# Kernel optimization log

Hardware: AMD Instinct MI355X
Metric: run time of the kernel (lower is better)

Reference implementation:

```python
import jax, jax.numpy as jnp
import numpy as np

B, N = 32, 64
ATTR, STATE, REL, GDIM = 4, 8, 4, 32
NF = 128

def _ln(x, w, b, eps=1e-5):
    mu = jnp.mean(x, axis=-1, keepdims=True)
    var = jnp.mean((x - mu) ** 2, axis=-1, keepdims=True)
    return (x - mu) * jax.lax.rsqrt(var + eps) * w + b

def setup_inputs() -> dict:
    key = jax.random.key(0)
    ks = iter(jax.random.split(key, 32))
    d = {}
    d['attrs'] = jax.random.normal(next(ks), (B, N, ATTR), jnp.float32)
    d['states'] = jax.random.normal(next(ks), (B, N, STATE), jnp.float32)
    d['actions'] = jnp.zeros((B, N, 4), jnp.float32)  # action=False, unused
    d['rel_attrs'] = jax.random.normal(next(ks), (B, N, N, REL), jnp.float32)
    def w(shape):
        return jax.random.normal(next(ks), shape, jnp.float32) * 0.05
    d['oe_w0'] = w((NF, ATTR + STATE)); d['oe_b0'] = jnp.zeros((NF,), jnp.float32)
    d['oe_w1'] = w((NF, NF));            d['oe_b1'] = jnp.zeros((NF,), jnp.float32)
    d['re_w0'] = w((NF, STATE + REL + 2 * ATTR)); d['re_b0'] = jnp.zeros((NF,), jnp.float32)
    d['re_w1'] = w((NF, NF));            d['re_b1'] = jnp.zeros((NF,), jnp.float32)
    d['rp_w'] = w((NF, NF + 2 * NF));    d['rp_b'] = jnp.zeros((NF,), jnp.float32)
    d['rp_lnw'] = jnp.ones((NF,), jnp.float32); d['rp_lnb'] = jnp.zeros((NF,), jnp.float32)
    d['pp_w'] = w((NF, 2 * NF));         d['pp_b'] = jnp.zeros((NF,), jnp.float32)
    d['pp_lnw'] = jnp.ones((NF,), jnp.float32); d['pp_lnb'] = jnp.zeros((NF,), jnp.float32)
    d['pr_w0'] = w((NF, NF));            d['pr_b0'] = jnp.zeros((NF,), jnp.float32)
    d['pr_w1'] = w((GDIM, NF));          d['pr_b1'] = jnp.zeros((GDIM,), jnp.float32)
    d['pstep'] = 2
    return d

def reference(attrs, states, actions, rel_attrs,
              oe_w0, oe_b0, oe_w1, oe_b1,
              re_w0, re_b0, re_w1, re_b1,
              rp_w, rp_b, rp_lnw, rp_lnb,
              pp_w, pp_b, pp_lnw, pp_lnb,
              pr_w0, pr_b0, pr_w1, pr_b1, pstep):
    lin = lambda x, w, b: jnp.einsum('...i,oi->...o', x, w) + b
    # ---- encode nodes: [B,N,attr+state] -> [B,N,NF] (action=False) ----
    obj_in = jnp.concatenate([attrs, states], axis=2)
    obj_encode = jax.nn.relu(lin(jax.nn.relu(lin(obj_in, oe_w0, oe_b0)), oe_w1, oe_b1))
    # ---- encode edges over dense N x N pairs ----
    rel_states = states[:, :, None, :] - states[:, None, :, :]        # B,N,N,state
    recv_attr = jnp.broadcast_to(attrs[:, :, None, :], (attrs.shape[0], attrs.shape[1], attrs.shape[1], attrs.shape[2]))
    send_attr = jnp.broadcast_to(attrs[:, None, :, :], recv_attr.shape)
    rel_in = jnp.concatenate([rel_attrs, rel_states, recv_attr, send_attr], axis=3)
    rel_encode = jax.nn.relu(lin(jax.nn.relu(lin(rel_in, re_w0, re_b0)), re_w1, re_b1))  # B,N,N,NF
    # ---- propagation steps ----
    for _ in range(pstep):
        sh = rel_encode.shape[:3] + (obj_encode.shape[-1],)
        recv = jnp.broadcast_to(obj_encode[:, :, None, :], sh)
        send = jnp.broadcast_to(obj_encode[:, None, :, :], sh)
        rel_effect = jax.nn.relu(_ln(lin(jnp.concatenate([rel_encode, recv, send], axis=3), rp_w, rp_b), rp_lnw, rp_lnb))
        rel_agg = rel_effect.sum(axis=2)                               # B,N,NF
        obj_encode = jax.nn.relu(_ln(lin(jnp.concatenate([obj_encode, rel_agg], axis=2), pp_w, pp_b), pp_lnw, pp_lnb))
    # ---- predict + tanh (state_encoder has tanh=True) ----
    out = lin(jax.nn.relu(lin(obj_encode, pr_w0, pr_b0)), pr_w1, pr_b1)
    return jnp.tanh(out)
```

## Files before the change

kernel.cpp:

```cpp
#include <hip/hip_runtime.h>


#define ROWS 2048
typedef unsigned short u16;
typedef unsigned int u32;
typedef __attribute__((ext_vector_type(8))) short bf16x8;
typedef __attribute__((ext_vector_type(4))) float f32x4;

__device__ __forceinline__ float bsu(u16 u) { return __uint_as_float(((u32)u) << 16); }
__device__ __forceinline__ u16 f2b(float f) {
    u32 u = __float_as_uint(f);
    u32 r = (u + 0x7fffu + ((u >> 16) & 1u)) >> 16;
    return (u16)r;
}

__global__ __launch_bounds__(256)
void k_prep(const float* __restrict__ re_w1, const float* __restrict__ rp_w,
            const float* __restrict__ oe_w1, const float* __restrict__ pp_w,
            const float* __restrict__ pr_w0, const float* __restrict__ pr_w1,
            u16* __restrict__ wbfA, u16* __restrict__ wbfB,
            u16* __restrict__ oe_w1b, u16* __restrict__ wrecvb, u16* __restrict__ wsendb,
            u16* __restrict__ pp_wb, u16* __restrict__ pr_w0b, u16* __restrict__ pr_w1b)
{
    int idx = blockIdx.x * 256 + threadIdx.x;
    if (idx < 17408) { int r = idx / 136, c = idx - r * 136;
        wbfA[idx] = f2b(c < 128 ? re_w1[r * 128 + c] : 0.f); return; }
    idx -= 17408;
    if (idx < 17408) { int r = idx / 136, c = idx - r * 136;
        wbfB[idx] = f2b(c < 128 ? rp_w[r * 384 + c] : 0.f); return; }
    idx -= 17408;
    if (idx < 16384) { oe_w1b[idx] = f2b(oe_w1[idx]); return; }
    idx -= 16384;
    if (idx < 16384) { int r = idx >> 7, c = idx & 127;
        wrecvb[idx] = f2b(rp_w[r * 384 + 128 + c]); return; }
    idx -= 16384;
    if (idx < 16384) { int r = idx >> 7, c = idx & 127;
        wsendb[idx] = f2b(rp_w[r * 384 + 256 + c]); return; }
    idx -= 16384;
    if (idx < 32768) { pp_wb[idx] = f2b(pp_w[idx]); return; }
    idx -= 32768;
    if (idx < 16384) { pr_w0b[idx] = f2b(pr_w0[idx]); return; }
    idx -= 16384;
    if (idx < 4096)  { pr_w1b[idx] = f2b(pr_w1[idx]); }
}

__global__ __launch_bounds__(256)
void k_node(const float* __restrict__ attrs, const float* __restrict__ states,
            const float* __restrict__ oe_w0, const float* __restrict__ oe_b0,
            const u16* __restrict__ oe_w1b, const float* __restrict__ oe_b1,
            const float* __restrict__ re_w0, const float* __restrict__ re_b0,
            const u16* __restrict__ wrecvb, const u16* __restrict__ wsendb,
            const float* __restrict__ rp_b,
            u16* __restrict__ objb, float* __restrict__ nr, float* __restrict__ ns,
            float* __restrict__ recvT, float* __restrict__ sendT)
{
    const int r0 = blockIdx.x * 16;
    const int t = threadIdx.x;
    __shared__ float xs[16][12];
    __shared__ float w0s[1536];
    __shared__ float rw0s[2560];
    __shared__ __align__(16) u16 hb[16 * 136];
    __shared__ __align__(16) u16 ob[16 * 136];

    if (t < 192) { int row = t / 12, c = t - row * 12;
        xs[row][c] = (c < 4) ? attrs[(r0 + row) * 4 + c] : states[(r0 + row) * 8 + (c - 4)]; }
    for (int i = t; i < 1536; i += 256) w0s[i] = oe_w0[i];
    for (int i = t; i < 2560; i += 256) rw0s[i] = re_w0[i];
    __syncthreads();

    for (int e = t; e < 2048; e += 256) {
        int row = e >> 7, o = e & 127;
        float h = oe_b0[o];
#pragma unroll
        for (int k = 0; k < 12; k++) h += w0s[o * 12 + k] * xs[row][k];
        hb[row * 136 + o] = f2b(fmaxf(h, 0.f));
        float s0 = 0.f, a0 = 0.f, a1 = 0.f;
#pragma unroll
        for (int k = 0; k < 8; k++) s0 += rw0s[o * 20 + 4 + k] * xs[row][4 + k];
#pragma unroll
        for (int k = 0; k < 4; k++) {
            a0 += rw0s[o * 20 + 12 + k] * xs[row][k];
            a1 += rw0s[o * 20 + 16 + k] * xs[row][k];
        }
        nr[(r0 + row) * 128 + o] = s0 + a0 + re_b0[o];
        ns[(r0 + row) * 128 + o] = a1 - s0;
    }
    __syncthreads();

    const int wave = t >> 6, lane = t & 63, tx = lane & 15, quad = lane >> 4;

    bf16x8 afr[4];
#pragma unroll
    for (int kk = 0; kk < 4; kk++) afr[kk] = *(const bf16x8*)&hb[tx * 136 + kk * 32 + quad * 8];
    f32x4 acc[2]; acc[0] = (f32x4){0.f,0.f,0.f,0.f}; acc[1] = acc[0];
#pragma unroll
    for (int ot = 0; ot < 2; ot++) {
        int o = (wave * 2 + ot) * 16 + tx;
#pragma unroll
        for (int kk = 0; kk < 4; kk++) {
            bf16x8 bfr = *(const bf16x8*)&oe_w1b[o * 128 + kk * 32 + quad * 8];
            acc[ot] = __builtin_amdgcn_mfma_f32_16x16x32_bf16(afr[kk], bfr, acc[ot], 0, 0, 0);
        }
    }
#pragma unroll
    for (int ot = 0; ot < 2; ot++) {
        int o = (wave * 2 + ot) * 16 + tx;
        float bia = oe_b1[o];
#pragma unroll
        for (int r = 0; r < 4; r++)
            ob[(quad * 4 + r) * 136 + o] = f2b(fmaxf(acc[ot][r] + bia, 0.f));
    }
    __syncthreads();
    { int m = t >> 4, c = t & 15;
      *(uint4*)&objb[(r0 + m) * 128 + c * 8] = *(const uint4*)&ob[m * 136 + c * 8]; }

#pragma unroll
    for (int kk = 0; kk < 4; kk++) afr[kk] = *(const bf16x8*)&ob[tx * 136 + kk * 32 + quad * 8];
    f32x4 ar[2], an[2];
    ar[0] = (f32x4){0.f,0.f,0.f,0.f}; ar[1] = ar[0]; an[0] = ar[0]; an[1] = ar[0];
#pragma unroll
    for (int ot = 0; ot < 2; ot++) {
        int o = (wave * 2 + ot) * 16 + tx;
#pragma unroll
        for (int kk = 0; kk < 4; kk++) {
            bf16x8 br = *(const bf16x8*)&wrecvb[o * 128 + kk * 32 + quad * 8];
            ar[ot] = __builtin_amdgcn_mfma_f32_16x16x32_bf16(afr[kk], br, ar[ot], 0, 0, 0);
            bf16x8 bs = *(const bf16x8*)&wsendb[o * 128 + kk * 32 + quad * 8];
            an[ot] = __builtin_amdgcn_mfma_f32_16x16x32_bf16(afr[kk], bs, an[ot], 0, 0, 0);
        }
    }
#pragma unroll
    for (int ot = 0; ot < 2; ot++) {
        int o = (wave * 2 + ot) * 16 + tx;
        float rb = rp_b[o];
#pragma unroll
        for (int r = 0; r < 4; r++) {
            recvT[(r0 + quad * 4 + r) * 128 + o] = ar[ot][r] + rb;
            sendT[(r0 + quad * 4 + r) * 128 + o] = an[ot][r];
        }
    }
}

__global__ __launch_bounds__(256)
void k_edge_enc(const float* __restrict__ rel_attrs,
                const float* __restrict__ re_w0, const u16* __restrict__ wbf,
                const float* __restrict__ re_b1,
                const float* __restrict__ nr, const float* __restrict__ ns,
                u16* __restrict__ relE)
{
    const int blk = blockIdx.x;
    const int b = blk >> 6;
    const int t = threadIdx.x;
    __shared__ __align__(16) u16 wlds[128 * 136];
    __shared__ __align__(16) u16 albuf[64 * 136];
    __shared__ float nrs[128];
    __shared__ float w0a[128][4];
    __shared__ float ras[64][4];

    {
        const uint4* src = (const uint4*)wbf;
        uint4* dst = (uint4*)wlds;
        for (int i = t; i < 2176; i += 256) dst[i] = src[i];
    }
    if (t < 128) {
        nrs[t] = nr[blk * 128 + t];
#pragma unroll
        for (int c = 0; c < 4; c++) w0a[t][c] = re_w0[t * 20 + c];
    } else {
        int j = t - 128;
        if (j < 64) {
#pragma unroll
            for (int c = 0; c < 4; c++) ras[j][c] = rel_attrs[(blk * 64 + j) * 4 + c];
        }
    }
    __syncthreads();

    for (int e = t; e < 64 * 128; e += 256) {
        int j = e >> 7, o = e & 127;
        float v = nrs[o] + ns[(b * 64 + j) * 128 + o];
#pragma unroll
        for (int c = 0; c < 4; c++) v += w0a[o][c] * ras[j][c];
        albuf[j * 136 + o] = f2b(fmaxf(v, 0.f));
    }
    __syncthreads();

    const int wave = t >> 6, lane = t & 63;
    const int tx = lane & 15, quad = lane >> 4;

    bf16x8 afr[4];
#pragma unroll
    for (int kk = 0; kk < 4; kk++)
        afr[kk] = *(const bf16x8*)&albuf[(wave * 16 + tx) * 136 + kk * 32 + quad * 8];

    f32x4 acc[8];
#pragma unroll
    for (int oo = 0; oo < 8; oo++) acc[oo] = (f32x4){0.f, 0.f, 0.f, 0.f};

#pragma unroll
    for (int oo = 0; oo < 8; oo++) {
        const int o = oo * 16 + tx;
        bf16x8 bfr[4];
#pragma unroll
        for (int kk = 0; kk < 4; kk++)
            bfr[kk] = *(const bf16x8*)&wlds[o * 136 + kk * 32 + quad * 8];
#pragma unroll
        for (int kk = 0; kk < 4; kk++)
            acc[oo] = __builtin_amdgcn_mfma_f32_16x16x32_bf16(afr[kk], bfr[kk], acc[oo], 0, 0, 0);
    }
    __syncthreads();

    u16* stg = albuf;
#pragma unroll
    for (int oo = 0; oo < 8; oo++) {
        const int o = oo * 16 + tx;
        float bia = re_b1[o];
#pragma unroll
        for (int r = 0; r < 4; r++)
            stg[(wave * 16 + quad * 4 + r) * 128 + o] = f2b(fmaxf(acc[oo][r] + bia, 0.f));
    }
    __syncthreads();
    {
        const uint4* src = (const uint4*)stg;
        uint4* dst = (uint4*)(relE + (size_t)blk * 64 * 128);
        for (int i = t; i < 1024; i += 256) dst[i] = src[i];
    }
}

__global__ __launch_bounds__(256)
void k_prop_edge(const u16* __restrict__ relE, const u16* __restrict__ wbf,
                 const float* __restrict__ rp_lnw, const float* __restrict__ rp_lnb,
                 const float* __restrict__ recvT, const float* __restrict__ sendT,
                 u16* __restrict__ aggb)
{
    const int blk = blockIdx.x;
    const int b = blk >> 6;
    const int t = threadIdx.x;
    __shared__ __align__(16) u16 wlds[128 * 136];
    __shared__ __align__(16) u16 albuf[64 * 136];
    __shared__ float lnws[128], lnbs[128];

    {
        const uint4* src = (const uint4*)wbf;
        uint4* dst = (uint4*)wlds;
        for (int i = t; i < 2176; i += 256) dst[i] = src[i];
    }
    {
        const uint4* src = (const uint4*)(relE + (size_t)blk * 64 * 128);
        for (int i = t; i < 1024; i += 256) {
            int r = i >> 4, c = i & 15;
            *(uint4*)&albuf[r * 136 + c * 8] = src[i];
        }
    }
    if (t < 128) { lnws[t] = rp_lnw[t]; lnbs[t] = rp_lnb[t]; }
    __syncthreads();

    const int wave = t >> 6, lane = t & 63;
    const int tx = lane & 15, quad = lane >> 4;

    bf16x8 afr[4];
#pragma unroll
    for (int kk = 0; kk < 4; kk++)
        afr[kk] = *(const bf16x8*)&albuf[(wave * 16 + tx) * 136 + kk * 32 + quad * 8];

    f32x4 acc[8];
#pragma unroll
    for (int oo = 0; oo < 8; oo++) acc[oo] = (f32x4){0.f, 0.f, 0.f, 0.f};

#pragma unroll
    for (int oo = 0; oo < 8; oo++) {
        const int o = oo * 16 + tx;
        bf16x8 bfr[4];
#pragma unroll
        for (int kk = 0; kk < 4; kk++)
            bfr[kk] = *(const bf16x8*)&wlds[o * 136 + kk * 32 + quad * 8];
#pragma unroll
        for (int kk = 0; kk < 4; kk++)
            acc[oo] = __builtin_amdgcn_mfma_f32_16x16x32_bf16(afr[kk], bfr[kk], acc[oo], 0, 0, 0);
    }

    const int jrow = wave * 16 + quad * 4;
#pragma unroll
    for (int oo = 0; oo < 8; oo++) {
        const int o = oo * 16 + tx;
        float rv = recvT[blk * 128 + o];
#pragma unroll
        for (int r = 0; r < 4; r++)
            acc[oo][r] += rv + sendT[(b * 64 + jrow + r) * 128 + o];
    }

    float s[4], q[4];
#pragma unroll
    for (int r = 0; r < 4; r++) {
        s[r] = 0.f; q[r] = 0.f;
#pragma unroll
        for (int oo = 0; oo < 8; oo++) { s[r] += acc[oo][r]; q[r] += acc[oo][r] * acc[oo][r]; }
    }
#pragma unroll
    for (int m = 1; m < 16; m <<= 1) {
#pragma unroll
        for (int r = 0; r < 4; r++) {
            s[r] += __shfl_xor(s[r], m, 64);
            q[r] += __shfl_xor(q[r], m, 64);
        }
    }
    float mu[4], rs[4];
#pragma unroll
    for (int r = 0; r < 4; r++) {
        mu[r] = s[r] * (1.f / 128.f);
        float var = q[r] * (1.f / 128.f) - mu[r] * mu[r];
        rs[r] = rsqrtf(var + 1e-5f);
    }

    float pa[8];
#pragma unroll
    for (int oo = 0; oo < 8; oo++) {
        const int o = oo * 16 + tx;
        float lw = lnws[o], lb = lnbs[o];
        float p = 0.f;
#pragma unroll
        for (int r = 0; r < 4; r++) {
            float z = (acc[oo][r] - mu[r]) * rs[r] * lw + lb;
            p += fmaxf(z, 0.f);
        }
        pa[oo] = p;
    }
    __syncthreads();

    float* scr = (float*)albuf;
    const int g = wave * 4 + quad;
#pragma unroll
    for (int oo = 0; oo < 8; oo++) scr[g * 132 + oo * 16 + tx] = pa[oo];
    __syncthreads();
    if (t < 128) {
        float sum = 0.f;
#pragma unroll
        for (int gg = 0; gg < 16; gg++) sum += scr[gg * 132 + t];
        aggb[blk * 128 + t] = f2b(sum);
    }
}

__global__ __launch_bounds__(256)
void k_prop_node(const u16* __restrict__ aggb,
                 const u16* __restrict__ pp_wb, const float* __restrict__ pp_b,
                 const float* __restrict__ pp_lnw, const float* __restrict__ pp_lnb,
                 const u16* __restrict__ wrecvb, const u16* __restrict__ wsendb,
                 const float* __restrict__ rp_b,
                 u16* __restrict__ objb, float* __restrict__ recvT, float* __restrict__ sendT,
                 int compute_terms)
{
    const int r0 = blockIdx.x * 16;
    const int t = threadIdx.x;
    __shared__ __align__(16) u16 ab[16 * 264];
    __shared__ __align__(16) u16 ob[16 * 136];
    __shared__ float redS[64], redQ[64];

    for (int i = t; i < 512; i += 256) {
        int m = i >> 5, c = i & 31;
        uint4 v = (c < 16) ? *(const uint4*)&objb[(r0 + m) * 128 + (c & 15) * 8]
                           : *(const uint4*)&aggb[(r0 + m) * 128 + (c - 16) * 8];
        *(uint4*)&ab[m * 264 + c * 8] = v;
    }
    __syncthreads();

    const int wave = t >> 6, lane = t & 63, tx = lane & 15, quad = lane >> 4;
    bf16x8 afr[8];
#pragma unroll
    for (int kk = 0; kk < 8; kk++) afr[kk] = *(const bf16x8*)&ab[tx * 264 + kk * 32 + quad * 8];
    f32x4 acc[2]; acc[0] = (f32x4){0.f,0.f,0.f,0.f}; acc[1] = acc[0];
#pragma unroll
    for (int ot = 0; ot < 2; ot++) {
        int o = (wave * 2 + ot) * 16 + tx;
#pragma unroll
        for (int kk = 0; kk < 8; kk++) {
            bf16x8 bfr = *(const bf16x8*)&pp_wb[o * 256 + kk * 32 + quad * 8];
            acc[ot] = __builtin_amdgcn_mfma_f32_16x16x32_bf16(afr[kk], bfr, acc[ot], 0, 0, 0);
        }
    }
#pragma unroll
    for (int ot = 0; ot < 2; ot++) {
        float bia = pp_b[(wave * 2 + ot) * 16 + tx];
#pragma unroll
        for (int r = 0; r < 4; r++) acc[ot][r] += bia;
    }

    float s[4], q[4];
#pragma unroll
    for (int r = 0; r < 4; r++) {
        s[r] = acc[0][r] + acc[1][r];
        q[r] = acc[0][r] * acc[0][r] + acc[1][r] * acc[1][r];
    }
#pragma unroll
    for (int m = 1; m < 16; m <<= 1) {
#pragma unroll
        for (int r = 0; r < 4; r++) {
            s[r] += __shfl_xor(s[r], m, 64);
            q[r] += __shfl_xor(q[r], m, 64);
        }
    }
    if (tx == 0) {
#pragma unroll
        for (int r = 0; r < 4; r++) {
            redS[wave * 16 + quad * 4 + r] = s[r];
            redQ[wave * 16 + quad * 4 + r] = q[r];
        }
    }
    __syncthreads();
    float mu[4], rs[4];
#pragma unroll
    for (int r = 0; r < 4; r++) {
        int m = quad * 4 + r;
        float ss = redS[m] + redS[16 + m] + redS[32 + m] + redS[48 + m];
        float qq = redQ[m] + redQ[16 + m] + redQ[32 + m] + redQ[48 + m];
        mu[r] = ss * (1.f / 128.f);
        rs[r] = rsqrtf(qq * (1.f / 128.f) - mu[r] * mu[r] + 1e-5f);
    }
#pragma unroll
    for (int ot = 0; ot < 2; ot++) {
        int o = (wave * 2 + ot) * 16 + tx;
        float lw = pp_lnw[o], lb = pp_lnb[o];
#pragma unroll
        for (int r = 0; r < 4; r++) {
            float z = (acc[ot][r] - mu[r]) * rs[r] * lw + lb;
            ob[(quad * 4 + r) * 136 + o] = f2b(fmaxf(z, 0.f));
        }
    }
    __syncthreads();
    { int m = t >> 4, c = t & 15;
      *(uint4*)&objb[(r0 + m) * 128 + c * 8] = *(const uint4*)&ob[m * 136 + c * 8]; }

    if (compute_terms) {
        bf16x8 af2[4];
#pragma unroll
        for (int kk = 0; kk < 4; kk++) af2[kk] = *(const bf16x8*)&ob[tx * 136 + kk * 32 + quad * 8];
        f32x4 ar[2], an[2];
        ar[0] = (f32x4){0.f,0.f,0.f,0.f}; ar[1] = ar[0]; an[0] = ar[0]; an[1] = ar[0];
#pragma unroll
        for (int ot = 0; ot < 2; ot++) {
            int o = (wave * 2 + ot) * 16 + tx;
#pragma unroll
            for (int kk = 0; kk < 4; kk++) {
                bf16x8 br = *(const bf16x8*)&wrecvb[o * 128 + kk * 32 + quad * 8];
                ar[ot] = __builtin_amdgcn_mfma_f32_16x16x32_bf16(af2[kk], br, ar[ot], 0, 0, 0);
                bf16x8 bs = *(const bf16x8*)&wsendb[o * 128 + kk * 32 + quad * 8];
                an[ot] = __builtin_amdgcn_mfma_f32_16x16x32_bf16(af2[kk], bs, an[ot], 0, 0, 0);
            }
        }
#pragma unroll
        for (int ot = 0; ot < 2; ot++) {
            int o = (wave * 2 + ot) * 16 + tx;
            float rb = rp_b[o];
#pragma unroll
            for (int r = 0; r < 4; r++) {
                recvT[(r0 + quad * 4 + r) * 128 + o] = ar[ot][r] + rb;
                sendT[(r0 + quad * 4 + r) * 128 + o] = an[ot][r];
            }
        }
    }
}

__global__ __launch_bounds__(256)
void k_predict(const u16* __restrict__ objb,
               const u16* __restrict__ pr_w0b, const float* __restrict__ pr_b0,
               const u16* __restrict__ pr_w1b, const float* __restrict__ pr_b1,
               float* __restrict__ out)
{
    const int r0 = blockIdx.x * 16;
    const int t = threadIdx.x;
    __shared__ __align__(16) u16 ab[16 * 136];
    __shared__ __align__(16) u16 hb2[16 * 136];
    { int m = t >> 4, c = t & 15;
      *(uint4*)&ab[m * 136 + c * 8] = *(const uint4*)&objb[(r0 + m) * 128 + c * 8]; }
    __syncthreads();

    const int wave = t >> 6, lane = t & 63, tx = lane & 15, quad = lane >> 4;
    bf16x8 afr[4];
#pragma unroll
    for (int kk = 0; kk < 4; kk++) afr[kk] = *(const bf16x8*)&ab[tx * 136 + kk * 32 + quad * 8];
    f32x4 acc[2]; acc[0] = (f32x4){0.f,0.f,0.f,0.f}; acc[1] = acc[0];
#pragma unroll
    for (int ot = 0; ot < 2; ot++) {
        int o = (wave * 2 + ot) * 16 + tx;
#pragma unroll
        for (int kk = 0; kk < 4; kk++) {
            bf16x8 bfr = *(const bf16x8*)&pr_w0b[o * 128 + kk * 32 + quad * 8];
            acc[ot] = __builtin_amdgcn_mfma_f32_16x16x32_bf16(afr[kk], bfr, acc[ot], 0, 0, 0);
        }
    }
#pragma unroll
    for (int ot = 0; ot < 2; ot++) {
        int o = (wave * 2 + ot) * 16 + tx;
        float bia = pr_b0[o];
#pragma unroll
        for (int r = 0; r < 4; r++)
            hb2[(quad * 4 + r) * 136 + o] = f2b(fmaxf(acc[ot][r] + bia, 0.f));
    }
    __syncthreads();
    if (wave < 2) {
        bf16x8 af2[4];
#pragma unroll
        for (int kk = 0; kk < 4; kk++) af2[kk] = *(const bf16x8*)&hb2[tx * 136 + kk * 32 + quad * 8];
        f32x4 a2 = (f32x4){0.f,0.f,0.f,0.f};
        int o = wave * 16 + tx;
#pragma unroll
        for (int kk = 0; kk < 4; kk++) {
            bf16x8 bfr = *(const bf16x8*)&pr_w1b[o * 128 + kk * 32 + quad * 8];
            a2 = __builtin_amdgcn_mfma_f32_16x16x32_bf16(af2[kk], bfr, a2, 0, 0, 0);
        }
        float bia = pr_b1[o];
#pragma unroll
        for (int r = 0; r < 4; r++)
            out[(r0 + quad * 4 + r) * 32 + o] = tanhf(a2[r] + bia);
    }
}

extern "C" void kernel_launch(void* const* d_in, const int* in_sizes, int n_in,
                              void* d_out, int out_size, void* d_ws, size_t ws_size,
                              hipStream_t stream)
{
    const float* attrs    = (const float*)d_in[0];
    const float* states   = (const float*)d_in[1];
    const float* rel_attrs= (const float*)d_in[3];
    const float* oe_w0 = (const float*)d_in[4];
    const float* oe_b0 = (const float*)d_in[5];
    const float* oe_w1 = (const float*)d_in[6];
    const float* oe_b1 = (const float*)d_in[7];
    const float* re_w0 = (const float*)d_in[8];
    const float* re_b0 = (const float*)d_in[9];
    const float* re_w1 = (const float*)d_in[10];
    const float* re_b1 = (const float*)d_in[11];
    const float* rp_w  = (const float*)d_in[12];
    const float* rp_b  = (const float*)d_in[13];
    const float* rp_lnw= (const float*)d_in[14];
    const float* rp_lnb= (const float*)d_in[15];
    const float* pp_w  = (const float*)d_in[16];
    const float* pp_b  = (const float*)d_in[17];
    const float* pp_lnw= (const float*)d_in[18];
    const float* pp_lnb= (const float*)d_in[19];
    const float* pr_w0 = (const float*)d_in[20];
    const float* pr_b0 = (const float*)d_in[21];
    const float* pr_w1 = (const float*)d_in[22];
    const float* pr_b1 = (const float*)d_in[23];

    float* ws    = (float*)d_ws;
    float* nr    = ws;
    float* ns    = nr    + ROWS * 128;
    float* recvT = ns    + ROWS * 128;
    float* sendT = recvT + ROWS * 128;
    u16* wbfA   = (u16*)(sendT + ROWS * 128);
    u16* wbfB   = wbfA + 17408;
    u16* oe_w1b = wbfB + 17408;
    u16* wrecvb = oe_w1b + 16384;
    u16* wsendb = wrecvb + 16384;
    u16* pp_wb  = wsendb + 16384;
    u16* pr_w0b = pp_wb + 32768;
    u16* pr_w1b = pr_w0b + 16384;
    u16* objb   = pr_w1b + 4096;
    u16* aggb   = objb + ROWS * 128;
    u16* relE   = aggb + ROWS * 128;

    k_prep<<<536, 256, 0, stream>>>(re_w1, rp_w, oe_w1, pp_w, pr_w0, pr_w1,
                                    wbfA, wbfB, oe_w1b, wrecvb, wsendb,
                                    pp_wb, pr_w0b, pr_w1b);
    k_node<<<128, 256, 0, stream>>>(attrs, states, oe_w0, oe_b0, oe_w1b, oe_b1,
                                    re_w0, re_b0, wrecvb, wsendb, rp_b,
                                    objb, nr, ns, recvT, sendT);
    k_edge_enc<<<2048, 256, 0, stream>>>(rel_attrs, re_w0, wbfA, re_b1, nr, ns, relE);
    for (int p = 0; p < 2; p++) {
        k_prop_edge<<<2048, 256, 0, stream>>>(relE, wbfB, rp_lnw, rp_lnb, recvT, sendT, aggb);
        k_prop_node<<<128, 256, 0, stream>>>(aggb, pp_wb, pp_b, pp_lnw, pp_lnb,
                                             wrecvb, wsendb, rp_b,
                                             objb, recvT, sendT, (p == 0) ? 1 : 0);
    }
    k_predict<<<128, 256, 0, stream>>>(objb, pr_w0b, pr_b0, pr_w1b, pr_b1, (float*)d_out);
}
```

Baseline: 209.2 us.

## Persist edge blocks over four row groups and store edges in MFMA fragment layout

```diff
diff --git a/kernel.cpp b/kernel.cpp
--- a/kernel.cpp
+++ b/kernel.cpp
@@ -7,7 +7,6 @@
 typedef __attribute__((ext_vector_type(8))) short bf16x8;
 typedef __attribute__((ext_vector_type(4))) float f32x4;
 
-__device__ __forceinline__ float bsu(u16 u) { return __uint_as_float(((u32)u) << 16); }
 __device__ __forceinline__ u16 f2b(float f) {
     u32 u = __float_as_uint(f);
     u32 r = (u + 0x7fffu + ((u >> 16) & 1u)) >> 16;
@@ -23,12 +22,12 @@
             u16* __restrict__ pp_wb, u16* __restrict__ pr_w0b, u16* __restrict__ pr_w1b)
 {
     int idx = blockIdx.x * 256 + threadIdx.x;
-    if (idx < 17408) { int r = idx / 136, c = idx - r * 136;
+    if (idx < 18432) { int r = idx / 144, c = idx - r * 144;
         wbfA[idx] = f2b(c < 128 ? re_w1[r * 128 + c] : 0.f); return; }
-    idx -= 17408;
-    if (idx < 17408) { int r = idx / 136, c = idx - r * 136;
+    idx -= 18432;
+    if (idx < 18432) { int r = idx / 144, c = idx - r * 144;
         wbfB[idx] = f2b(c < 128 ? rp_w[r * 384 + c] : 0.f); return; }
-    idx -= 17408;
+    idx -= 18432;
     if (idx < 16384) { oe_w1b[idx] = f2b(oe_w1[idx]); return; }
     idx -= 16384;
     if (idx < 16384) { int r = idx >> 7, c = idx & 127;
@@ -146,13 +145,11 @@
                 const float* __restrict__ re_w0, const u16* __restrict__ wbf,
                 const float* __restrict__ re_b1,
                 const float* __restrict__ nr, const float* __restrict__ ns,
-                u16* __restrict__ relE)
-{
-    const int blk = blockIdx.x;
-    const int b = blk >> 6;
+                u16* __restrict__ relEF)
+{
     const int t = threadIdx.x;
-    __shared__ __align__(16) u16 wlds[128 * 136];
-    __shared__ __align__(16) u16 albuf[64 * 136];
+    __shared__ __align__(16) u16 wlds[128 * 144];
+    __shared__ __align__(16) u16 hsb[64 * 144];
     __shared__ float nrs[128];
     __shared__ float w0a[128][4];
     __shared__ float ras[64][4];
@@ -160,182 +157,170 @@
     {
         const uint4* src = (const uint4*)wbf;
         uint4* dst = (uint4*)wlds;
-        for (int i = t; i < 2176; i += 256) dst[i] = src[i];
+        for (int i = t; i < 2304; i += 256) dst[i] = src[i];
     }
     if (t < 128) {
-        nrs[t] = nr[blk * 128 + t];
 #pragma unroll
         for (int c = 0; c < 4; c++) w0a[t][c] = re_w0[t * 20 + c];
-    } else {
-        int j = t - 128;
-        if (j < 64) {
-#pragma unroll
-            for (int c = 0; c < 4; c++) ras[j][c] = rel_attrs[(blk * 64 + j) * 4 + c];
-        }
-    }
-    __syncthreads();
-
-    for (int e = t; e < 64 * 128; e += 256) {
-        int j = e >> 7, o = e & 127;
-        float v = nrs[o] + ns[(b * 64 + j) * 128 + o];
-#pragma unroll
-        for (int c = 0; c < 4; c++) v += w0a[o][c] * ras[j][c];
-        albuf[j * 136 + o] = f2b(fmaxf(v, 0.f));
-    }
-    __syncthreads();
-
-    const int wave = t >> 6, lane = t & 63;
-    const int tx = lane & 15, quad = lane >> 4;
-
-    bf16x8 afr[4];
-#pragma unroll
-    for (int kk = 0; kk < 4; kk++)
-        afr[kk] = *(const bf16x8*)&albuf[(wave * 16 + tx) * 136 + kk * 32 + quad * 8];
-
-    f32x4 acc[8];
-#pragma unroll
-    for (int oo = 0; oo < 8; oo++) acc[oo] = (f32x4){0.f, 0.f, 0.f, 0.f};
-
-#pragma unroll
-    for (int oo = 0; oo < 8; oo++) {
-        const int o = oo * 16 + tx;
-        bf16x8 bfr[4];
+    }
+    const int wave = t >> 6, lane = t & 63, tx = lane & 15, quad = lane >> 4;
+
+    for (int g = 0; g < 4; g++) {
+        const int blkg = blockIdx.x * 4 + g;
+        const int b = blkg >> 6;
+        __syncthreads();
+        if (t < 128) nrs[t] = nr[blkg * 128 + t];
+        else if (t < 192) {
+            int j = t - 128;
+#pragma unroll
+            for (int c = 0; c < 4; c++) ras[j][c] = rel_attrs[(blkg * 64 + j) * 4 + c];
+        }
+        __syncthreads();
+
+        for (int e = t; e < 64 * 128; e += 256) {
+            int j = e >> 7, o = e & 127;
+            float v = nrs[o] + ns[(b * 64 + j) * 128 + o];
+#pragma unroll
+            for (int c = 0; c < 4; c++) v += w0a[o][c] * ras[j][c];
+            hsb[j * 144 + o] = f2b(fmaxf(v, 0.f));
+        }
+        __syncthreads();
+
+        bf16x8 afr[4];
 #pragma unroll
         for (int kk = 0; kk < 4; kk++)
-            bfr[kk] = *(const bf16x8*)&wlds[o * 136 + kk * 32 + quad * 8];
-#pragma unroll
-        for (int kk = 0; kk < 4; kk++)
-            acc[oo] = __builtin_amdgcn_mfma_f32_16x16x32_bf16(afr[kk], bfr[kk], acc[oo], 0, 0, 0);
-    }
-    __syncthreads();
-
-    u16* stg = albuf;
-#pragma unroll
-    for (int oo = 0; oo < 8; oo++) {
-        const int o = oo * 16 + tx;
-        float bia = re_b1[o];
-#pragma unroll
-        for (int r = 0; r < 4; r++)
-            stg[(wave * 16 + quad * 4 + r) * 128 + o] = f2b(fmaxf(acc[oo][r] + bia, 0.f));
-    }
-    __syncthreads();
-    {
-        const uint4* src = (const uint4*)stg;
-        uint4* dst = (uint4*)(relE + (size_t)blk * 64 * 128);
-        for (int i = t; i < 1024; i += 256) dst[i] = src[i];
+            afr[kk] = *(const bf16x8*)&hsb[(wave * 16 + tx) * 144 + kk * 32 + quad * 8];
+
+        f32x4 acc[8];
+#pragma unroll
+        for (int oo = 0; oo < 8; oo++) acc[oo] = (f32x4){0.f, 0.f, 0.f, 0.f};
+#pragma unroll
+        for (int oo = 0; oo < 8; oo++) {
+            const int o = oo * 16 + tx;
+#pragma unroll
+            for (int kk = 0; kk < 4; kk++) {
+                bf16x8 bfr = *(const bf16x8*)&wlds[o * 144 + kk * 32 + quad * 8];
+                acc[oo] = __builtin_amdgcn_mfma_f32_16x16x32_bf16(afr[kk], bfr, acc[oo], 0, 0, 0);
+            }
+        }
+        __syncthreads();
+
+#pragma unroll
+        for (int oo = 0; oo < 8; oo++) {
+            const int o = oo * 16 + tx;
+            float bia = re_b1[o];
+#pragma unroll
+            for (int r = 0; r < 4; r++)
+                hsb[(wave * 16 + quad * 4 + r) * 144 + o] = f2b(fmaxf(acc[oo][r] + bia, 0.f));
+        }
+#pragma unroll
+        for (int kt = 0; kt < 4; kt++) {
+            bf16x8 v = *(const bf16x8*)&hsb[(wave * 16 + tx) * 144 + kt * 32 + quad * 8];
+            *(bf16x8*)(relEF + ((size_t)((blkg * 4 + wave) * 4 + kt) * 64 + lane) * 8) = v;
+        }
     }
 }
 
 __global__ __launch_bounds__(256)
-void k_prop_edge(const u16* __restrict__ relE, const u16* __restrict__ wbf,
+void k_prop_edge(const u16* __restrict__ relEF, const u16* __restrict__ wbf,
                  const float* __restrict__ rp_lnw, const float* __restrict__ rp_lnb,
                  const float* __restrict__ recvT, const float* __restrict__ sendT,
                  u16* __restrict__ aggb)
 {
-    const int blk = blockIdx.x;
-    const int b = blk >> 6;
     const int t = threadIdx.x;
-    __shared__ __align__(16) u16 wlds[128 * 136];
-    __shared__ __align__(16) u16 albuf[64 * 136];
+    __shared__ __align__(16) u16 wlds[128 * 144];
+    __shared__ float scr[16 * 132];
     __shared__ float lnws[128], lnbs[128];
 
     {
         const uint4* src = (const uint4*)wbf;
         uint4* dst = (uint4*)wlds;
-        for (int i = t; i < 2176; i += 256) dst[i] = src[i];
-    }
-    {
-        const uint4* src = (const uint4*)(relE + (size_t)blk * 64 * 128);
-        for (int i = t; i < 1024; i += 256) {
-            int r = i >> 4, c = i & 15;
-            *(uint4*)&albuf[r * 136 + c * 8] = src[i];
-        }
+        for (int i = t; i < 2304; i += 256) dst[i] = src[i];
     }
     if (t < 128) { lnws[t] = rp_lnw[t]; lnbs[t] = rp_lnb[t]; }
     __syncthreads();
 
-    const int wave = t >> 6, lane = t & 63;
-    const int tx = lane & 15, quad = lane >> 4;
-
-    bf16x8 afr[4];
-#pragma unroll
-    for (int kk = 0; kk < 4; kk++)
-        afr[kk] = *(const bf16x8*)&albuf[(wave * 16 + tx) * 136 + kk * 32 + quad * 8];
-
-    f32x4 acc[8];
-#pragma unroll
-    for (int oo = 0; oo < 8; oo++) acc[oo] = (f32x4){0.f, 0.f, 0.f, 0.f};
-
-#pragma unroll
-    for (int oo = 0; oo < 8; oo++) {
-        const int o = oo * 16 + tx;
-        bf16x8 bfr[4];
-#pragma unroll
-        for (int kk = 0; kk < 4; kk++)
-            bfr[kk] = *(const bf16x8*)&wlds[o * 136 + kk * 32 + quad * 8];
-#pragma unroll
-        for (int kk = 0; kk < 4; kk++)
-            acc[oo] = __builtin_amdgcn_mfma_f32_16x16x32_bf16(afr[kk], bfr[kk], acc[oo], 0, 0, 0);
-    }
-
-    const int jrow = wave * 16 + quad * 4;
-#pragma unroll
-    for (int oo = 0; oo < 8; oo++) {
-        const int o = oo * 16 + tx;
-        float rv = recvT[blk * 128 + o];
-#pragma unroll
-        for (int r = 0; r < 4; r++)
-            acc[oo][r] += rv + sendT[(b * 64 + jrow + r) * 128 + o];
-    }
-
-    float s[4], q[4];
-#pragma unroll
-    for (int r = 0; r < 4; r++) {
-        s[r] = 0.f; q[r] = 0.f;
-#pragma unroll
-        for (int oo = 0; oo < 8; oo++) { s[r] += acc[oo][r]; q[r] += acc[oo][r] * acc[oo][r]; }
-    }
-#pragma unroll
-    for (int m = 1; m < 16; m <<= 1) {
+    const int wave = t >> 6, lane = t & 63, tx = lane & 15, quad = lane >> 4;
+
+    for (int g = 0; g < 4; g++) {
+        const int blkg = blockIdx.x * 4 + g;
+        const int b = blkg >> 6;
+
+        bf16x8 afr[4];
+#pragma unroll
+        for (int kt = 0; kt < 4; kt++)
+            afr[kt] = *(const bf16x8*)(relEF + ((size_t)((blkg * 4 + wave) * 4 + kt) * 64 + lane) * 8);
+
+        f32x4 acc[8];
+#pragma unroll
+        for (int oo = 0; oo < 8; oo++) acc[oo] = (f32x4){0.f, 0.f, 0.f, 0.f};
+#pragma unroll
+        for (int oo = 0; oo < 8; oo++) {
+            const int o = oo * 16 + tx;
+#pragma unroll
+            for (int kk = 0; kk < 4; kk++) {
+                bf16x8 bfr = *(const bf16x8*)&wlds[o * 144 + kk * 32 + quad * 8];
+                acc[oo] = __builtin_amdgcn_mfma_f32_16x16x32_bf16(afr[kk], bfr, acc[oo], 0, 0, 0);
+            }
+        }
+
+        const int jrow = wave * 16 + quad * 4;
+#pragma unroll
+        for (int oo = 0; oo < 8; oo++) {
+            const int o = oo * 16 + tx;
+            float rv = recvT[blkg * 128 + o];
+#pragma unroll
+            for (int r = 0; r < 4; r++)
+                acc[oo][r] += rv + sendT[(b * 64 + jrow + r) * 128 + o];
+        }
+
+        float s[4], q[4];
 #pragma unroll
         for (int r = 0; r < 4; r++) {
-            s[r] += __shfl_xor(s[r], m, 64);
-            q[r] += __shfl_xor(q[r], m, 64);
-        }
-    }
-    float mu[4], rs[4];
-#pragma unroll
-    for (int r = 0; r < 4; r++) {
-        mu[r] = s[r] * (1.f / 128.f);
-        float var = q[r] * (1.f / 128.f) - mu[r] * mu[r];
-        rs[r] = rsqrtf(var + 1e-5f);
-    }
-
-    float pa[8];
-#pragma unroll
-    for (int oo = 0; oo < 8; oo++) {
-        const int o = oo * 16 + tx;
-        float lw = lnws[o], lb = lnbs[o];
-        float p = 0.f;
+            s[r] = 0.f; q[r] = 0.f;
+#pragma unroll
+            for (int oo = 0; oo < 8; oo++) { s[r] += acc[oo][r]; q[r] += acc[oo][r] * acc[oo][r]; }
+        }
+#pragma unroll
+        for (int m = 1; m < 16; m <<= 1) {
+#pragma unroll
+            for (int r = 0; r < 4; r++) {
+                s[r] += __shfl_xor(s[r], m, 64);
+                q[r] += __shfl_xor(q[r], m, 64);
+            }
+        }
+        float mu[4], rs[4];
 #pragma unroll
         for (int r = 0; r < 4; r++) {
-            float z = (acc[oo][r] - mu[r]) * rs[r] * lw + lb;
-            p += fmaxf(z, 0.f);
-        }
-        pa[oo] = p;
-    }
-    __syncthreads();
-
-    float* scr = (float*)albuf;
-    const int g = wave * 4 + quad;
-#pragma unroll
-    for (int oo = 0; oo < 8; oo++) scr[g * 132 + oo * 16 + tx] = pa[oo];
-    __syncthreads();
-    if (t < 128) {
-        float sum = 0.f;
-#pragma unroll
-        for (int gg = 0; gg < 16; gg++) sum += scr[gg * 132 + t];
-        aggb[blk * 128 + t] = f2b(sum);
+            mu[r] = s[r] * (1.f / 128.f);
+            float var = q[r] * (1.f / 128.f) - mu[r] * mu[r];
+            rs[r] = rsqrtf(var + 1e-5f);
+        }
+
+        float pa[8];
+#pragma unroll
+        for (int oo = 0; oo < 8; oo++) {
+            const int o = oo * 16 + tx;
+            float lw = lnws[o], lb = lnbs[o];
+            float p = 0.f;
+#pragma unroll
+            for (int r = 0; r < 4; r++) {
+                float z = (acc[oo][r] - mu[r]) * rs[r] * lw + lb;
+                p += fmaxf(z, 0.f);
+            }
+            pa[oo] = p;
+        }
+        __syncthreads();
+        const int grp = wave * 4 + quad;
+#pragma unroll
+        for (int oo = 0; oo < 8; oo++) scr[grp * 132 + oo * 16 + tx] = pa[oo];
+        __syncthreads();
+        if (t < 128) {
+            float sum = 0.f;
+#pragma unroll
+            for (int gg = 0; gg < 16; gg++) sum += scr[gg * 132 + t];
+            aggb[blkg * 128 + t] = f2b(sum);
+        }
     }
 }
 
@@ -547,8 +532,8 @@
     float* recvT = ns    + ROWS * 128;
     float* sendT = recvT + ROWS * 128;
     u16* wbfA   = (u16*)(sendT + ROWS * 128);
-    u16* wbfB   = wbfA + 17408;
-    u16* oe_w1b = wbfB + 17408;
+    u16* wbfB   = wbfA + 18432;
+    u16* oe_w1b = wbfB + 18432;
     u16* wrecvb = oe_w1b + 16384;
     u16* wsendb = wrecvb + 16384;
     u16* pp_wb  = wsendb + 16384;
@@ -556,17 +541,17 @@
     u16* pr_w1b = pr_w0b + 16384;
     u16* objb   = pr_w1b + 4096;
     u16* aggb   = objb + ROWS * 128;
-    u16* relE   = aggb + ROWS * 128;
-
-    k_prep<<<536, 256, 0, stream>>>(re_w1, rp_w, oe_w1, pp_w, pr_w0, pr_w1,
+    u16* relEF  = aggb + ROWS * 128;
+
+    k_prep<<<544, 256, 0, stream>>>(re_w1, rp_w, oe_w1, pp_w, pr_w0, pr_w1,
                                     wbfA, wbfB, oe_w1b, wrecvb, wsendb,
                                     pp_wb, pr_w0b, pr_w1b);
     k_node<<<128, 256, 0, stream>>>(attrs, states, oe_w0, oe_b0, oe_w1b, oe_b1,
                                     re_w0, re_b0, wrecvb, wsendb, rp_b,
                                     objb, nr, ns, recvT, sendT);
-    k_edge_enc<<<2048, 256, 0, stream>>>(rel_attrs, re_w0, wbfA, re_b1, nr, ns, relE);
+    k_edge_enc<<<512, 256, 0, stream>>>(rel_attrs, re_w0, wbfA, re_b1, nr, ns, relEF);
     for (int p = 0; p < 2; p++) {
-        k_prop_edge<<<2048, 256, 0, stream>>>(relE, wbfB, rp_lnw, rp_lnb, recvT, sendT, aggb);
+        k_prop_edge<<<512, 256, 0, stream>>>(relEF, wbfB, rp_lnw, rp_lnb, recvT, sendT, aggb);
         k_prop_node<<<128, 256, 0, stream>>>(aggb, pp_wb, pp_b, pp_lnw, pp_lnb,
                                              wrecvb, wsendb, rp_b,
                                              objb, recvT, sendT, (p == 0) ? 1 : 0);
```

Result: faster. 199.6 us (-4.6%).
